# Optimization experiments

Measured on AMD Instinct MI355X. Metric: run time of the kernel, lower is better.

The kernel has to match this reference:

```python
import jax, jax.numpy as jnp
import numpy as np

DIM = 128     # output_dim
HID = 256     # hidden_dim
MAX_N = 64
B = 8192
LN_EPS = 1e-5

def _ln(h, g, b):
    mu = h.mean(-1, keepdims=True)
    v = ((h - mu) ** 2).mean(-1, keepdims=True)
    return (h - mu) / jnp.sqrt(v + LN_EPS) * g + b

def setup_inputs():
    key = jax.random.key(0)
    ks = jax.random.split(key, 8)
    def p(k, shape, fan_in):
        return jax.random.normal(k, shape, jnp.float32) / np.float32(np.sqrt(fan_in))
    KM = (MAX_N + HID) // 2   # 160, key_net mid
    DM = (HID + DIM) // 2     # 192, decoder mid
    SM = (HID + 1) // 2       # 128, size_pred mid
    return {
        "z": jax.random.normal(ks[0], (B, HID), jnp.float32),
        "kW1": p(ks[1], (MAX_N, KM), MAX_N), "kb1": jnp.zeros((KM,), jnp.float32),
        "kg": jnp.ones((KM,), jnp.float32), "kbe": jnp.zeros((KM,), jnp.float32),
        "kW2": p(ks[2], (KM, HID), KM), "kb2": jnp.zeros((HID,), jnp.float32),
        "dW1": p(ks[3], (HID, DM), HID), "db1": jnp.zeros((DM,), jnp.float32),
        "dW2": p(ks[4], (DM, DIM), DM), "db2": jnp.zeros((DIM,), jnp.float32),
        "sW1": p(ks[5], (HID, SM), HID), "sb1": jnp.zeros((SM,), jnp.float32),
        "sg": jnp.ones((SM,), jnp.float32), "sbe": jnp.zeros((SM,), jnp.float32),
        "sW2": p(ks[6], (SM, 1), SM), "sb2": jnp.zeros((1,), jnp.float32),
    }

def reference(z, kW1, kb1, kg, kbe, kW2, kb2, dW1, db1, dW2, db2,
              sW1, sb1, sg, sbe, sW2, sb2):
    # size_pred MLP (Linear -> LN -> ReLU -> Linear): [B, 1]
    h = jax.nn.relu(_ln(z @ sW1 + sb1, sg, sbe))
    n_logits = h @ sW2 + sb2
    n = jnp.clip(jnp.round(n_logits[:, 0]).astype(jnp.int32), 0, MAX_N - 1)  # [B]
    # onehot positional encodings for all slots 0..MAX_N-1 -> keys via key_net
    pos = jnp.eye(MAX_N, dtype=z.dtype)                          # [MAX_N, MAX_N]
    keys = jnp.tanh(_ln(pos @ kW1 + kb1, kg, kbe)) @ kW2 + kb2   # [MAX_N, HID]
    # dense form of repeat_interleave + ragged arange: zp[b, j] = z[b] * keys[j]
    zp = z[:, None, :] * keys[None, :, :]                        # [B, MAX_N, HID]
    x = jnp.tanh(zp @ dW1 + db1) @ dW2 + db2                     # [B, MAX_N, DIM]
    mask = jnp.arange(MAX_N)[None, :] < n[:, None]               # [B, MAX_N] valid slots
    # masked dense output; rows where mask is True correspond exactly to the
    # torch ragged output (x, batch) in row-major order
    return x * mask[:, :, None], n_logits, n
```

## Files before the change

kernel.cpp:

```cpp
#include <hip/hip_runtime.h>
#include <math.h>

#define B_SZ 8192
#define HID 256
#define DIM 128
#define MAXN 64
#define KM 160
#define DM 192
#define SM 128
#define LN_EPS 1e-5f

#define SP_BLOCKS 256
#define SP_BATCH 32
#define ZPAD 36

__global__ void __launch_bounds__(256) sp_keys_kernel(
    const float* __restrict__ z,
    const float* __restrict__ kW1, const float* __restrict__ kb1,
    const float* __restrict__ kg,  const float* __restrict__ kbe,
    const float* __restrict__ kW2, const float* __restrict__ kb2,
    const float* __restrict__ sW1, const float* __restrict__ sb1,
    const float* __restrict__ sg,  const float* __restrict__ sbe,
    const float* __restrict__ sW2, const float* __restrict__ sb2,
    float* __restrict__ out_logits, float* __restrict__ out_nf,
    int* __restrict__ n_ws, float* __restrict__ keys)
{
    __shared__ float smem[HID * ZPAD];
    const int blk = blockIdx.x;
    const int tid = threadIdx.x;

    if (blk >= SP_BLOCKS) {
        const int j = blk - SP_BLOCKS;
        float* red = smem;
        float* t_s = smem + 256;

        float v = 0.f;
        if (tid < KM) v = kW1[j * KM + tid] + kb1[tid];

        red[tid] = (tid < KM) ? v : 0.f;
        __syncthreads();
        for (int s = 128; s > 0; s >>= 1) {
            if (tid < s) red[tid] += red[tid + s];
            __syncthreads();
        }
        const float mu = red[0] / (float)KM;
        __syncthreads();

        const float d = (tid < KM) ? (v - mu) : 0.f;
        red[tid] = d * d;
        __syncthreads();
        for (int s = 128; s > 0; s >>= 1) {
            if (tid < s) red[tid] += red[tid + s];
            __syncthreads();
        }
        const float rstd = rsqrtf(red[0] / (float)KM + LN_EPS);
        __syncthreads();

        if (tid < KM) t_s[tid] = tanhf(d * rstd * kg[tid] + kbe[tid]);
        __syncthreads();

        float acc = kb2[tid];
        #pragma unroll 4
        for (int k = 0; k < KM; ++k) acc = fmaf(t_s[k], kW2[k * HID + tid], acc);
        keys[j * HID + tid] = acc;
        return;
    }

    float (*z_s)[ZPAD] = (float(*)[ZPAD])smem;
    const int b0 = blk * SP_BATCH;

    {
        const float4* z4 = (const float4*)z;
        #pragma unroll
        for (int i = 0; i < 8; ++i) {
            const int idx = tid + 256 * i;
            const int r = idx >> 6, c4 = idx & 63;
            const float4 v = z4[(size_t)(b0 + r) * 64 + c4];
            z_s[4 * c4 + 0][r] = v.x;
            z_s[4 * c4 + 1][r] = v.y;
            z_s[4 * c4 + 2][r] = v.z;
            z_s[4 * c4 + 3][r] = v.w;
        }
    }
    __syncthreads();

    const int cq = tid & 31;
    const int bg = tid >> 5;

    float acc[4][4];
    #pragma unroll
    for (int bi = 0; bi < 4; ++bi)
        #pragma unroll
        for (int ci = 0; ci < 4; ++ci) acc[bi][ci] = 0.f;

    const float4* w4p = (const float4*)sW1;
    #pragma unroll 4
    for (int k = 0; k < HID; ++k) {
        const float4 wv = w4p[k * 32 + cq];
        const float4 zb = *(const float4*)&z_s[k][bg * 4];
        const float zz[4] = {zb.x, zb.y, zb.z, zb.w};
        const float ww[4] = {wv.x, wv.y, wv.z, wv.w};
        #pragma unroll
        for (int bi = 0; bi < 4; ++bi)
            #pragma unroll
            for (int ci = 0; ci < 4; ++ci)
                acc[bi][ci] = fmaf(zz[bi], ww[ci], acc[bi][ci]);
    }

    const float4 g4v  = ((const float4*)sg)[cq];
    const float4 be4v = ((const float4*)sbe)[cq];
    const float4 w24v = ((const float4*)sW2)[cq];
    const float g4[4]  = {g4v.x, g4v.y, g4v.z, g4v.w};
    const float be4[4] = {be4v.x, be4v.y, be4v.z, be4v.w};
    const float w24[4] = {w24v.x, w24v.y, w24v.z, w24v.w};
    const float sb2v = sb2[0];
    const float b1_0 = sb1[4 * cq + 0], b1_1 = sb1[4 * cq + 1],
                b1_2 = sb1[4 * cq + 2], b1_3 = sb1[4 * cq + 3];

    #pragma unroll
    for (int bi = 0; bi < 4; ++bi) {
        float a[4] = {acc[bi][0] + b1_0, acc[bi][1] + b1_1,
                      acc[bi][2] + b1_2, acc[bi][3] + b1_3};
        float s = a[0] + a[1] + a[2] + a[3];
        #pragma unroll
        for (int off = 1; off < 32; off <<= 1) s += __shfl_xor(s, off, 64);
        const float mu = s * (1.f / (float)SM);
        float d[4], vs = 0.f;
        #pragma unroll
        for (int ci = 0; ci < 4; ++ci) { d[ci] = a[ci] - mu; vs = fmaf(d[ci], d[ci], vs); }
        #pragma unroll
        for (int off = 1; off < 32; off <<= 1) vs += __shfl_xor(vs, off, 64);
        const float rstd = rsqrtf(vs * (1.f / (float)SM) + LN_EPS);

        float p = 0.f;
        #pragma unroll
        for (int ci = 0; ci < 4; ++ci) {
            float h = fmaf(d[ci] * rstd, g4[ci], be4[ci]);
            h = fmaxf(h, 0.f);
            p = fmaf(h, w24[ci], p);
        }
        #pragma unroll
        for (int off = 1; off < 32; off <<= 1) p += __shfl_xor(p, off, 64);

        if (cq == 0) {
            const int b = b0 + bg * 4 + bi;
            const float logit = p + sb2v;
            int n = (int)rintf(logit);
            n = min(max(n, 0), MAXN - 1);
            out_logits[b] = logit;
            out_nf[b] = (float)n;
            n_ws[b] = n;
        }
    }
}

__global__ void __launch_bounds__(256) mega_kernel(
    const float* __restrict__ z, const float* __restrict__ keys,
    const int* __restrict__ n_ws,
    const float* __restrict__ dW1, const float* __restrict__ db1,
    const float* __restrict__ dW2, const float* __restrict__ db2,
    float* __restrict__ out0)
{
    __shared__ __align__(16) float z_s[4][HID];
    __shared__ __align__(16) float s_s[HID][4];
    __shared__ __align__(16) float t_s[DM][4];
    __shared__ __align__(16) float pbuf[4 * DM * 4];
    __shared__ int n_s[4];
    __shared__ int rlist[4 * (MAXN - 1)];

    const int blk = blockIdx.x;
    const int tid = threadIdx.x;
    const int w = tid >> 6, lane = tid & 63;
    const int b0 = blk * 4;

    if (tid < 4) n_s[tid] = n_ws[b0 + tid];
    __syncthreads();

    const float4 zf = make_float4(0.f, 0.f, 0.f, 0.f);
    #pragma unroll
    for (int bi = 0; bi < 4; ++bi) {
        const int n = n_s[bi];
        float4* o4 = (float4*)(out0 + (size_t)(b0 + bi) * (MAXN * DIM)) + n * 32;
        const int cnt4 = (MAXN - n) * 32;
        for (int idx = tid; idx < cnt4; idx += 256) o4[idx] = zf;
    }

    const int total = n_s[0] + n_s[1] + n_s[2] + n_s[3];
    if (total == 0) return;

    {
        const int r = tid >> 6, c4 = tid & 63;
        ((float4*)z_s[r])[c4] = ((const float4*)(z + (size_t)(b0 + r) * HID))[c4];
    }
    if (tid < 4) {
        int off = 0;
        for (int i = 0; i < tid; ++i) off += n_s[i];
        for (int j = 0; j < n_s[tid]; ++j) rlist[off + j] = (tid << 6) | j;
    }
    __syncthreads();

    float (*hp)[DM][4]  = (float(*)[DM][4])pbuf;
    float (*op)[DIM][4] = (float(*)[DIM][4])pbuf;

    for (int base = 0; base < total; base += 4) {
        const int rcnt = min(4, total - base);
        int bs[4], js[4];
        #pragma unroll
        for (int r = 0; r < 4; ++r) {
            const int e = rlist[base + min(r, rcnt - 1)];
            bs[r] = e >> 6; js[r] = e & 63;
        }

        #pragma unroll
        for (int r = 0; r < 4; ++r)
            s_s[tid][r] = z_s[bs[r]][tid] * keys[js[r] * HID + tid];
        __syncthreads();

        if (lane < 48) {
            float a[4][4];
            #pragma unroll
            for (int r = 0; r < 4; ++r)
                #pragma unroll
                for (int c = 0; c < 4; ++c) a[r][c] = 0.f;
            const int k0 = w * 64;
            #pragma unroll 8
            for (int kk = 0; kk < 64; ++kk) {
                const int k = k0 + kk;
                const float4 wv = ((const float4*)dW1)[(size_t)k * 48 + lane];
                const float4 sv = *(const float4*)&s_s[k][0];
                const float sr[4] = {sv.x, sv.y, sv.z, sv.w};
                const float wc[4] = {wv.x, wv.y, wv.z, wv.w};
                #pragma unroll
                for (int r = 0; r < 4; ++r)
                    #pragma unroll
                    for (int c = 0; c < 4; ++c)
                        a[r][c] = fmaf(sr[r], wc[c], a[r][c]);
            }
            #pragma unroll
            for (int c = 0; c < 4; ++c)
                *(float4*)&hp[w][4 * lane + c][0] =
                    make_float4(a[0][c], a[1][c], a[2][c], a[3][c]);
        }
        __syncthreads();

        if (tid < DM) {
            const float4 p0 = *(const float4*)&hp[0][tid][0];
            const float4 p1 = *(const float4*)&hp[1][tid][0];
            const float4 p2 = *(const float4*)&hp[2][tid][0];
            const float4 p3 = *(const float4*)&hp[3][tid][0];
            const float bb = db1[tid];
            *(float4*)&t_s[tid][0] = make_float4(
                tanhf(p0.x + p1.x + p2.x + p3.x + bb),
                tanhf(p0.y + p1.y + p2.y + p3.y + bb),
                tanhf(p0.z + p1.z + p2.z + p3.z + bb),
                tanhf(p0.w + p1.w + p2.w + p3.w + bb));
        }
        __syncthreads();

        if (lane < 32) {
            float o[4][4];
            #pragma unroll
            for (int r = 0; r < 4; ++r)
                #pragma unroll
                for (int c = 0; c < 4; ++c) o[r][c] = 0.f;
            const int k1 = w * 48;
            #pragma unroll 8
            for (int kk = 0; kk < 48; ++kk) {
                const int k = k1 + kk;
                const float4 wv = ((const float4*)dW2)[(size_t)k * 32 + lane];
                const float4 tv = *(const float4*)&t_s[k][0];
                const float tr[4] = {tv.x, tv.y, tv.z, tv.w};
                const float wc[4] = {wv.x, wv.y, wv.z, wv.w};
                #pragma unroll
                for (int r = 0; r < 4; ++r)
                    #pragma unroll
                    for (int c = 0; c < 4; ++c)
                        o[r][c] = fmaf(tr[r], wc[c], o[r][c]);
            }
            #pragma unroll
            for (int c = 0; c < 4; ++c)
                *(float4*)&op[w][4 * lane + c][0] =
                    make_float4(o[0][c], o[1][c], o[2][c], o[3][c]);
        }
        __syncthreads();

        if (tid < DIM) {
            const float4 q0 = *(const float4*)&op[0][tid][0];
            const float4 q1 = *(const float4*)&op[1][tid][0];
            const float4 q2 = *(const float4*)&op[2][tid][0];
            const float4 q3 = *(const float4*)&op[3][tid][0];
            const float bb = db2[tid];
            const float ov[4] = {q0.x + q1.x + q2.x + q3.x + bb,
                                 q0.y + q1.y + q2.y + q3.y + bb,
                                 q0.z + q1.z + q2.z + q3.z + bb,
                                 q0.w + q1.w + q2.w + q3.w + bb};
            #pragma unroll
            for (int r = 0; r < 4; ++r)
                if (r < rcnt)
                    out0[((size_t)(b0 + bs[r]) * MAXN + js[r]) * DIM + tid] = ov[r];
        }
        __syncthreads();
    }
}

extern "C" void kernel_launch(void* const* d_in, const int* in_sizes, int n_in,
                              void* d_out, int out_size, void* d_ws, size_t ws_size,
                              hipStream_t stream)
{
    const float* z   = (const float*)d_in[0];
    const float* kW1 = (const float*)d_in[1];
    const float* kb1 = (const float*)d_in[2];
    const float* kg  = (const float*)d_in[3];
    const float* kbe = (const float*)d_in[4];
    const float* kW2 = (const float*)d_in[5];
    const float* kb2 = (const float*)d_in[6];
    const float* dW1 = (const float*)d_in[7];
    const float* db1 = (const float*)d_in[8];
    const float* dW2 = (const float*)d_in[9];
    const float* db2 = (const float*)d_in[10];
    const float* sW1 = (const float*)d_in[11];
    const float* sb1 = (const float*)d_in[12];
    const float* sg  = (const float*)d_in[13];
    const float* sbe = (const float*)d_in[14];
    const float* sW2 = (const float*)d_in[15];
    const float* sb2 = (const float*)d_in[16];

    float* out0       = (float*)d_out;
    float* out_logits = out0 + (size_t)B_SZ * MAXN * DIM;
    float* out_nf     = out_logits + B_SZ;

    float* keys = (float*)d_ws;
    int*   n_ws = (int*)((char*)d_ws + 65536);

    sp_keys_kernel<<<SP_BLOCKS + MAXN, 256, 0, stream>>>(
        z, kW1, kb1, kg, kbe, kW2, kb2,
        sW1, sb1, sg, sbe, sW2, sb2,
        out_logits, out_nf, n_ws, keys);

    mega_kernel<<<B_SZ / 4, 256, 0, stream>>>(
        z, keys, n_ws, dW1, db1, dW2, db2, out0);
}
```

Baseline: 83.76 us.

## Fuse size predictor, key net and decoder into one kernel per 32 rows

Merges the size-prediction/key kernel and the decoder kernel into a single launch where each block handles 32 batch rows. Each block recomputes the needed key vectors (up to its max n) into shared memory instead of reading a global keys buffer, and keeps n in shared memory. This removes a kernel launch and the global round trip for n and keys. In exchange every block redoes the key-net work, the grid drops from 2048 to 256 blocks, and shared memory per block grows a lot (roughly 100KB), which limits occupancy.

Measured after the change: 114.6 us. 36.8% more time.

```diff
diff --git a/kernel.cpp b/kernel.cpp
--- a/kernel.cpp
+++ b/kernel.cpp
@@ -10,11 +10,11 @@
 #define SM 128
 #define LN_EPS 1e-5f
 
-#define SP_BLOCKS 256
-#define SP_BATCH 32
+#define NB 32
+#define GRID_BLKS (B_SZ / NB)
 #define ZPAD 36
 
-__global__ void __launch_bounds__(256) sp_keys_kernel(
+__global__ void __launch_bounds__(256) uber_kernel(
     const float* __restrict__ z,
     const float* __restrict__ kW1, const float* __restrict__ kb1,
     const float* __restrict__ kg,  const float* __restrict__ kbe,
@@ -22,52 +22,23 @@
     const float* __restrict__ sW1, const float* __restrict__ sb1,
     const float* __restrict__ sg,  const float* __restrict__ sbe,
     const float* __restrict__ sW2, const float* __restrict__ sb2,
-    float* __restrict__ out_logits, float* __restrict__ out_nf,
-    int* __restrict__ n_ws, float* __restrict__ keys)
+    const float* __restrict__ dW1, const float* __restrict__ db1,
+    const float* __restrict__ dW2, const float* __restrict__ db2,
+    float* __restrict__ out0, float* __restrict__ out_logits,
+    float* __restrict__ out_nf)
 {
-    __shared__ float smem[HID * ZPAD];
+    __shared__ __align__(16) float z_s[HID][ZPAD];
+    __shared__ __align__(16) float keys_s[MAXN][HID];
+    __shared__ __align__(16) float s_s[HID][4];
+    __shared__ __align__(16) float t_s[DM][4];
+    __shared__ __align__(16) float pbuf[4 * DM * 4];
+    __shared__ int n_s[NB];
+    __shared__ unsigned short rlist[NB * (MAXN - 1)];
+
     const int blk = blockIdx.x;
     const int tid = threadIdx.x;
-
-    if (blk >= SP_BLOCKS) {
-        const int j = blk - SP_BLOCKS;
-        float* red = smem;
-        float* t_s = smem + 256;
-
-        float v = 0.f;
-        if (tid < KM) v = kW1[j * KM + tid] + kb1[tid];
-
-        red[tid] = (tid < KM) ? v : 0.f;
-        __syncthreads();
-        for (int s = 128; s > 0; s >>= 1) {
-            if (tid < s) red[tid] += red[tid + s];
-            __syncthreads();
-        }
-        const float mu = red[0] / (float)KM;
-        __syncthreads();
-
-        const float d = (tid < KM) ? (v - mu) : 0.f;
-        red[tid] = d * d;
-        __syncthreads();
-        for (int s = 128; s > 0; s >>= 1) {
-            if (tid < s) red[tid] += red[tid + s];
-            __syncthreads();
-        }
-        const float rstd = rsqrtf(red[0] / (float)KM + LN_EPS);
-        __syncthreads();
-
-        if (tid < KM) t_s[tid] = tanhf(d * rstd * kg[tid] + kbe[tid]);
-        __syncthreads();
-
-        float acc = kb2[tid];
-        #pragma unroll 4
-        for (int k = 0; k < KM; ++k) acc = fmaf(t_s[k], kW2[k * HID + tid], acc);
-        keys[j * HID + tid] = acc;
-        return;
-    }
-
-    float (*z_s)[ZPAD] = (float(*)[ZPAD])smem;
-    const int b0 = blk * SP_BATCH;
+    const int w = tid >> 6, lane = tid & 63;
+    const int b0 = blk * NB;
 
     {
         const float4* z4 = (const float4*)z;
@@ -84,120 +55,141 @@
     }
     __syncthreads();
 
-    const int cq = tid & 31;
-    const int bg = tid >> 5;
-
-    float acc[4][4];
-    #pragma unroll
-    for (int bi = 0; bi < 4; ++bi)
-        #pragma unroll
-        for (int ci = 0; ci < 4; ++ci) acc[bi][ci] = 0.f;
-
-    const float4* w4p = (const float4*)sW1;
-    #pragma unroll 4
-    for (int k = 0; k < HID; ++k) {
-        const float4 wv = w4p[k * 32 + cq];
-        const float4 zb = *(const float4*)&z_s[k][bg * 4];
-        const float zz[4] = {zb.x, zb.y, zb.z, zb.w};
-        const float ww[4] = {wv.x, wv.y, wv.z, wv.w};
+    {
+        const int cq = tid & 31;
+        const int bg = tid >> 5;
+
+        float acc[4][4];
         #pragma unroll
         for (int bi = 0; bi < 4; ++bi)
             #pragma unroll
-            for (int ci = 0; ci < 4; ++ci)
-                acc[bi][ci] = fmaf(zz[bi], ww[ci], acc[bi][ci]);
-    }
-
-    const float4 g4v  = ((const float4*)sg)[cq];
-    const float4 be4v = ((const float4*)sbe)[cq];
-    const float4 w24v = ((const float4*)sW2)[cq];
-    const float g4[4]  = {g4v.x, g4v.y, g4v.z, g4v.w};
-    const float be4[4] = {be4v.x, be4v.y, be4v.z, be4v.w};
-    const float w24[4] = {w24v.x, w24v.y, w24v.z, w24v.w};
-    const float sb2v = sb2[0];
-    const float b1_0 = sb1[4 * cq + 0], b1_1 = sb1[4 * cq + 1],
-                b1_2 = sb1[4 * cq + 2], b1_3 = sb1[4 * cq + 3];
-
-    #pragma unroll
-    for (int bi = 0; bi < 4; ++bi) {
-        float a[4] = {acc[bi][0] + b1_0, acc[bi][1] + b1_1,
-                      acc[bi][2] + b1_2, acc[bi][3] + b1_3};
-        float s = a[0] + a[1] + a[2] + a[3];
-        #pragma unroll
-        for (int off = 1; off < 32; off <<= 1) s += __shfl_xor(s, off, 64);
-        const float mu = s * (1.f / (float)SM);
-        float d[4], vs = 0.f;
-        #pragma unroll
-        for (int ci = 0; ci < 4; ++ci) { d[ci] = a[ci] - mu; vs = fmaf(d[ci], d[ci], vs); }
-        #pragma unroll
-        for (int off = 1; off < 32; off <<= 1) vs += __shfl_xor(vs, off, 64);
-        const float rstd = rsqrtf(vs * (1.f / (float)SM) + LN_EPS);
-
-        float p = 0.f;
-        #pragma unroll
-        for (int ci = 0; ci < 4; ++ci) {
-            float h = fmaf(d[ci] * rstd, g4[ci], be4[ci]);
-            h = fmaxf(h, 0.f);
-            p = fmaf(h, w24[ci], p);
-        }
-        #pragma unroll
-        for (int off = 1; off < 32; off <<= 1) p += __shfl_xor(p, off, 64);
-
-        if (cq == 0) {
-            const int b = b0 + bg * 4 + bi;
-            const float logit = p + sb2v;
-            int n = (int)rintf(logit);
-            n = min(max(n, 0), MAXN - 1);
-            out_logits[b] = logit;
-            out_nf[b] = (float)n;
-            n_ws[b] = n;
-        }
-    }
-}
-
-__global__ void __launch_bounds__(256) mega_kernel(
-    const float* __restrict__ z, const float* __restrict__ keys,
-    const int* __restrict__ n_ws,
-    const float* __restrict__ dW1, const float* __restrict__ db1,
-    const float* __restrict__ dW2, const float* __restrict__ db2,
-    float* __restrict__ out0)
-{
-    __shared__ __align__(16) float z_s[4][HID];
-    __shared__ __align__(16) float s_s[HID][4];
-    __shared__ __align__(16) float t_s[DM][4];
-    __shared__ __align__(16) float pbuf[4 * DM * 4];
-    __shared__ int n_s[4];
-    __shared__ int rlist[4 * (MAXN - 1)];
-
-    const int blk = blockIdx.x;
-    const int tid = threadIdx.x;
-    const int w = tid >> 6, lane = tid & 63;
-    const int b0 = blk * 4;
-
-    if (tid < 4) n_s[tid] = n_ws[b0 + tid];
+            for (int ci = 0; ci < 4; ++ci) acc[bi][ci] = 0.f;
+
+        const float4* w4p = (const float4*)sW1;
+        #pragma unroll 4
+        for (int k = 0; k < HID; ++k) {
+            const float4 wv = w4p[k * 32 + cq];
+            const float4 zb = *(const float4*)&z_s[k][bg * 4];
+            const float zz[4] = {zb.x, zb.y, zb.z, zb.w};
+            const float ww[4] = {wv.x, wv.y, wv.z, wv.w};
+            #pragma unroll
+            for (int bi = 0; bi < 4; ++bi)
+                #pragma unroll
+                for (int ci = 0; ci < 4; ++ci)
+                    acc[bi][ci] = fmaf(zz[bi], ww[ci], acc[bi][ci]);
+        }
+
+        const float4 g4v  = ((const float4*)sg)[cq];
+        const float4 be4v = ((const float4*)sbe)[cq];
+        const float4 w24v = ((const float4*)sW2)[cq];
+        const float g4[4]  = {g4v.x, g4v.y, g4v.z, g4v.w};
+        const float be4[4] = {be4v.x, be4v.y, be4v.z, be4v.w};
+        const float w24[4] = {w24v.x, w24v.y, w24v.z, w24v.w};
+        const float sb2v = sb2[0];
+        const float b1_0 = sb1[4 * cq + 0], b1_1 = sb1[4 * cq + 1],
+                    b1_2 = sb1[4 * cq + 2], b1_3 = sb1[4 * cq + 3];
+
+        #pragma unroll
+        for (int bi = 0; bi < 4; ++bi) {
+            float a[4] = {acc[bi][0] + b1_0, acc[bi][1] + b1_1,
+                          acc[bi][2] + b1_2, acc[bi][3] + b1_3};
+            float s = a[0] + a[1] + a[2] + a[3];
+            #pragma unroll
+            for (int off = 1; off < 32; off <<= 1) s += __shfl_xor(s, off, 64);
+            const float mu = s * (1.f / (float)SM);
+            float d[4], vs = 0.f;
+            #pragma unroll
+            for (int ci = 0; ci < 4; ++ci) { d[ci] = a[ci] - mu; vs = fmaf(d[ci], d[ci], vs); }
+            #pragma unroll
+            for (int off = 1; off < 32; off <<= 1) vs += __shfl_xor(vs, off, 64);
+            const float rstd = rsqrtf(vs * (1.f / (float)SM) + LN_EPS);
+
+            float p = 0.f;
+            #pragma unroll
+            for (int ci = 0; ci < 4; ++ci) {
+                float h = fmaf(d[ci] * rstd, g4[ci], be4[ci]);
+                h = fmaxf(h, 0.f);
+                p = fmaf(h, w24[ci], p);
+            }
+            #pragma unroll
+            for (int off = 1; off < 32; off <<= 1) p += __shfl_xor(p, off, 64);
+
+            if (cq == 0) {
+                const int bl = bg * 4 + bi;
+                const float logit = p + sb2v;
+                int n = (int)rintf(logit);
+                n = min(max(n, 0), MAXN - 1);
+                out_logits[b0 + bl] = logit;
+                out_nf[b0 + bl] = (float)n;
+                n_s[bl] = n;
+            }
+        }
+    }
     __syncthreads();
 
-    const float4 zf = make_float4(0.f, 0.f, 0.f, 0.f);
-    #pragma unroll
-    for (int bi = 0; bi < 4; ++bi) {
-        const int n = n_s[bi];
-        float4* o4 = (float4*)(out0 + (size_t)(b0 + bi) * (MAXN * DIM)) + n * 32;
-        const int cnt4 = (MAXN - n) * 32;
-        for (int idx = tid; idx < cnt4; idx += 256) o4[idx] = zf;
-    }
-
-    const int total = n_s[0] + n_s[1] + n_s[2] + n_s[3];
+    {
+        const float4 zf = make_float4(0.f, 0.f, 0.f, 0.f);
+        for (int bi = 0; bi < NB; ++bi) {
+            const int n = n_s[bi];
+            float4* o4 = (float4*)(out0 + (size_t)(b0 + bi) * (MAXN * DIM)) + n * 32;
+            const int cnt4 = (MAXN - n) * 32;
+            for (int idx = tid; idx < cnt4; idx += 256) o4[idx] = zf;
+        }
+    }
+
+    int total = 0, nmax = 0;
+    for (int i = 0; i < NB; ++i) {
+        const int nn = n_s[i];
+        total += nn;
+        nmax = max(nmax, nn);
+    }
     if (total == 0) return;
 
-    {
-        const int r = tid >> 6, c4 = tid & 63;
-        ((float4*)z_s[r])[c4] = ((const float4*)(z + (size_t)(b0 + r) * HID))[c4];
-    }
-    if (tid < 4) {
+    if (tid < NB) {
         int off = 0;
         for (int i = 0; i < tid; ++i) off += n_s[i];
-        for (int j = 0; j < n_s[tid]; ++j) rlist[off + j] = (tid << 6) | j;
+        const int nn = n_s[tid];
+        for (int j = 0; j < nn; ++j)
+            rlist[off + j] = (unsigned short)((tid << 6) | j);
     }
     __syncthreads();
+
+    {
+        float* red = pbuf;
+        float* t_k = (float*)t_s;
+        for (int j = 0; j < nmax; ++j) {
+            float v = 0.f;
+            if (tid < KM) v = kW1[j * KM + tid] + kb1[tid];
+
+            red[tid] = (tid < KM) ? v : 0.f;
+            __syncthreads();
+            for (int s = 128; s > 0; s >>= 1) {
+                if (tid < s) red[tid] += red[tid + s];
+                __syncthreads();
+            }
+            const float mu = red[0] / (float)KM;
+            __syncthreads();
+
+            const float d = (tid < KM) ? (v - mu) : 0.f;
+            red[tid] = d * d;
+            __syncthreads();
+            for (int s = 128; s > 0; s >>= 1) {
+                if (tid < s) red[tid] += red[tid + s];
+                __syncthreads();
+            }
+            const float rstd = rsqrtf(red[0] / (float)KM + LN_EPS);
+            __syncthreads();
+
+            if (tid < KM) t_k[tid] = tanhf(d * rstd * kg[tid] + kbe[tid]);
+            __syncthreads();
+
+            float acc = kb2[tid];
+            #pragma unroll 4
+            for (int k = 0; k < KM; ++k) acc = fmaf(t_k[k], kW2[k * HID + tid], acc);
+            keys_s[j][tid] = acc;
+            __syncthreads();
+        }
+    }
 
     float (*hp)[DM][4]  = (float(*)[DM][4])pbuf;
     float (*op)[DIM][4] = (float(*)[DIM][4])pbuf;
@@ -213,7 +205,7 @@
 
         #pragma unroll
         for (int r = 0; r < 4; ++r)
-            s_s[tid][r] = z_s[bs[r]][tid] * keys[js[r] * HID + tid];
+            s_s[tid][r] = z_s[tid][bs[r]] * keys_s[js[r]][tid];
         __syncthreads();
 
         if (lane < 48) {
@@ -329,14 +321,9 @@
     float* out_logits = out0 + (size_t)B_SZ * MAXN * DIM;
     float* out_nf     = out_logits + B_SZ;
 
-    float* keys = (float*)d_ws;
-    int*   n_ws = (int*)((char*)d_ws + 65536);
-
-    sp_keys_kernel<<<SP_BLOCKS + MAXN, 256, 0, stream>>>(
+    uber_kernel<<<GRID_BLKS, 256, 0, stream>>>(
         z, kW1, kb1, kg, kbe, kW2, kb2,
         sW1, sb1, sg, sbe, sW2, sb2,
-        out_logits, out_nf, n_ws, keys);
-
-    mega_kernel<<<B_SZ / 4, 256, 0, stream>>>(
-        z, keys, n_ws, dW1, db1, dW2, db2, out0);
+        dW1, db1, dW2, db2,
+        out0, out_logits, out_nf);
 }
```
